# Kernel optimization log

Hardware: AMD Instinct MI355X
Metric: run time of the kernel (lower is better)

Reference implementation:

```python
import jax, jax.numpy as jnp
import numpy as np

B, S, D = 4, 2048, 512
H = 8
HD = D // H  # 64


def setup_inputs() -> dict:
    key = jax.random.key(0)
    k1, k2, k3 = jax.random.split(key, 3)
    x = jax.random.normal(k1, (B, S, D), dtype=jnp.float32)
    w_qkv = jax.random.normal(k2, (3 * D, D), dtype=jnp.float32) * (D ** -0.5)
    w_out = jax.random.normal(k3, (D, D), dtype=jnp.float32) * (D ** -0.5)
    return {"x": x, "w_qkv": w_qkv, "w_out": w_out}


def reference(x, w_qkv, w_out):
    b, s, d = x.shape
    # qkv projection (no bias), split into q,k,v
    qkv = jnp.einsum('bsd,ed->bse', x, w_qkv)  # [b, s, 3*d]
    q, k, v = jnp.split(qkv, 3, axis=2)
    # [b, s, h*hd] -> [b, h, s, hd]
    def to_heads(t):
        return t.reshape(b, s, H, HD).transpose(0, 2, 1, 3)
    q, k, v = to_heads(q), to_heads(k), to_heads(v)
    # NOTE: original module only scales by sqrt(head_dim) when mask is given;
    # with mask=None softmax is over raw QK^T scores.
    scores = jnp.einsum('bnid,bnjd->bnij', q, k)  # [b, h, s, s]
    attn = jax.nn.softmax(scores, axis=-1)
    o = jnp.einsum('bnij,bnjd->bnid', attn, v)  # [b, h, s, hd]
    o = o.transpose(0, 2, 1, 3).reshape(b, s, d)
    # dropout is identity (eval / drop_prob=0)
    return jnp.einsum('bsd,ed->bse', o, w_out)
```

## Files before the change

kernel.cpp:

```cpp
#include <hip/hip_runtime.h>
#include <hip/hip_bf16.h>

constexpr int B_  = 4;
constexpr int S_  = 2048;
constexpr int D_  = 512;
constexpr int H_  = 8;
constexpr int HD_ = 64;
constexpr int M_  = B_ * S_;

constexpr float LOG2E = 1.4426950408889634f;

typedef __attribute__((ext_vector_type(8))) short short8v;
typedef __attribute__((ext_vector_type(8))) _Float16 half8v;
typedef __attribute__((ext_vector_type(8))) unsigned short ushort8v;
typedef __attribute__((ext_vector_type(4))) float float4v;
typedef __attribute__((ext_vector_type(16))) float float16v;

__device__ __forceinline__ unsigned short f2bf(float x) {
    unsigned u = __builtin_bit_cast(unsigned, x);
    u += 0x7fffu + ((u >> 16) & 1u);
    return (unsigned short)(u >> 16);
}
__device__ __forceinline__ float bf2f(unsigned short h) {
    return __builtin_bit_cast(float, ((unsigned)h) << 16);
}
__device__ __forceinline__ unsigned short f2h(float x) {
    return __builtin_bit_cast(unsigned short, (_Float16)x);
}
__device__ __forceinline__ float fast_exp2(float x) {
#if __has_builtin(__builtin_amdgcn_exp2f)
    return __builtin_amdgcn_exp2f(x);
#else
    return exp2f(x);
#endif
}
__device__ __forceinline__ unsigned pack_bf16_trunc(float lo, float hi) {
    const unsigned ulo = __builtin_bit_cast(unsigned, lo);
    const unsigned uhi = __builtin_bit_cast(unsigned, hi);
#if __has_builtin(__builtin_amdgcn_perm)
    return __builtin_amdgcn_perm(uhi, ulo, 0x07060302u);
#else
    return (uhi & 0xffff0000u) | (ulo >> 16);
#endif
}
__device__ __forceinline__ void gload_lds16(const void* g, void* lds) {
    __builtin_amdgcn_global_load_lds((const __attribute__((address_space(1))) unsigned*)g,
                                     (__attribute__((address_space(3))) unsigned*)lds, 16, 0, 0);
}

__global__ __launch_bounds__(256) void prepass(const float* __restrict__ x,
                                               const float* __restrict__ wqkv,
                                               const float* __restrict__ wout,
                                               unsigned short* __restrict__ Xf,
                                               unsigned short* __restrict__ Wf,
                                               unsigned short* __restrict__ Wob) {
    const int bid = blockIdx.x, t = threadIdx.x;
    if (bid < 2048) {
        const int flat = bid * 256 + t;
        const int m = flat >> 6, c = (flat & 63) * 8;
        const float4 a = *(const float4*)&x[(size_t)m * 512 + c];
        const float4 b = *(const float4*)&x[(size_t)m * 512 + c + 4];
        const float v[8] = {a.x, a.y, a.z, a.w, b.x, b.y, b.z, b.w};
        ushort8v o;
#pragma unroll
        for (int i = 0; i < 8; ++i) o[i] = f2h(v[i]);
        *(ushort8v*)&Xf[(size_t)m * 512 + c] = o;
    } else if (bid < 2048 + 384) {
        const int flat = (bid - 2048) * 256 + t;
        const int e = flat >> 6, c = (flat & 63) * 8;
        const float4 a = *(const float4*)&wqkv[(size_t)e * 512 + c];
        const float4 b = *(const float4*)&wqkv[(size_t)e * 512 + c + 4];
        const float v[8] = {a.x, a.y, a.z, a.w, b.x, b.y, b.z, b.w};
        ushort8v o;
#pragma unroll
        for (int i = 0; i < 8; ++i) o[i] = f2h(v[i]);
        *(ushort8v*)&Wf[(size_t)e * 512 + c] = o;
    } else {
        const int flat = (bid - 2432) * 256 + t;
        const int e = flat >> 6, c = (flat & 63) * 8;
        const float4 a = *(const float4*)&wout[(size_t)e * 512 + c];
        const float4 b = *(const float4*)&wout[(size_t)e * 512 + c + 4];
        const float v[8] = {a.x, a.y, a.z, a.w, b.x, b.y, b.z, b.w};
        ushort8v o;
#pragma unroll
        for (int i = 0; i < 8; ++i) o[i] = f2bf(v[i]);
        *(ushort8v*)&Wob[(size_t)e * 512 + c] = o;
    }
}

__global__ __launch_bounds__(256, 2) void gemm_qkv(const unsigned short* __restrict__ Xf,
                                                   const unsigned short* __restrict__ Wf,
                                                   unsigned short* __restrict__ Qf,
                                                   unsigned short* __restrict__ KH,
                                                   unsigned short* __restrict__ VT) {
    __shared__ unsigned short Asm[2][128 * 64];
    __shared__ unsigned short Bsm[2][128 * 64];
    const int t = threadIdx.x, wv = t >> 6, lane = t & 63;
    const int fm = lane & 15, fq = lane >> 4;
    const int bid0 = blockIdx.x + 12 * blockIdx.y;
    const int xcd = bid0 & 7, ii = bid0 >> 3;
    const int x  = ii % 12;
    const int m0 = ((ii / 12) * 8 + xcd) * 128;
    const int slice = x >> 2;
    const int e0 = (x & 3) * 128;
    const bool vblk = (slice == 2);
    const int wrow = (wv >> 1) * 64, wcol = (wv & 1) * 64;

    const unsigned short* Bbase = Wf + (size_t)(e0 + slice * 512) * 512;

    const int srow = t >> 3;
    const int skb0 = t & 7;

    float4v acc[4][4];
#pragma unroll
    for (int i = 0; i < 4; ++i)
#pragma unroll
        for (int j = 0; j < 4; ++j) acc[i][j] = (float4v){0.f, 0.f, 0.f, 0.f};

#pragma unroll
    for (int i = 0; i < 4; ++i) {
        const int row = srow + 32 * i;
        const int kb = skb0 ^ (row & 7);
        gload_lds16(Xf + (size_t)(m0 + row) * 512 + kb * 8,
                    &Asm[0][(wv * 64 + 256 * i) * 8]);
        gload_lds16(Bbase + (size_t)row * 512 + kb * 8,
                    &Bsm[0][(wv * 64 + 256 * i) * 8]);
    }

    for (int kk = 0; kk < 8; ++kk) {
        __syncthreads();

        if (kk + 1 < 8) {
            const int k0n = (kk + 1) * 64;
            const int nbuf = (kk + 1) & 1;
#pragma unroll
            for (int i = 0; i < 4; ++i) {
                const int row = srow + 32 * i;
                const int kb = skb0 ^ (row & 7);
                gload_lds16(Xf + (size_t)(m0 + row) * 512 + k0n + kb * 8,
                            &Asm[nbuf][(wv * 64 + 256 * i) * 8]);
                gload_lds16(Bbase + (size_t)row * 512 + k0n + kb * 8,
                            &Bsm[nbuf][(wv * 64 + 256 * i) * 8]);
            }
        }

        const int buf = kk & 1;
#pragma unroll
        for (int ks = 0; ks < 2; ++ks) {
            half8v af[4], bf[4];
#pragma unroll
            for (int mt = 0; mt < 4; ++mt) {
                const int row = wrow + mt * 16 + fm;
                af[mt] = *(const half8v*)&Asm[buf][row * 64 + 8 * ((4 * ks + fq) ^ (row & 7))];
            }
#pragma unroll
            for (int nt = 0; nt < 4; ++nt) {
                const int row = wcol + nt * 16 + fm;
                bf[nt] = *(const half8v*)&Bsm[buf][row * 64 + 8 * ((4 * ks + fq) ^ (row & 7))];
            }
            if (vblk) {
#pragma unroll
                for (int mt = 0; mt < 4; ++mt)
#pragma unroll
                    for (int nt = 0; nt < 4; ++nt)
                        acc[mt][nt] = __builtin_amdgcn_mfma_f32_16x16x32_f16(bf[nt], af[mt], acc[mt][nt], 0, 0, 0);
            } else {
#pragma unroll
                for (int mt = 0; mt < 4; ++mt)
#pragma unroll
                    for (int nt = 0; nt < 4; ++nt)
                        acc[mt][nt] = __builtin_amdgcn_mfma_f32_16x16x32_f16(af[mt], bf[nt], acc[mt][nt], 0, 0, 0);
            }
        }
    }

    if (!vblk) {
        unsigned short* __restrict__ dst = (slice == 0) ? Qf : KH;
        const float sc = (slice == 0) ? LOG2E : 1.0f;
#pragma unroll
        for (int mt = 0; mt < 4; ++mt)
#pragma unroll
            for (int nt = 0; nt < 4; ++nt) {
                const int e = e0 + wcol + nt * 16 + fm;
                const int h = e >> 6, hd = e & 63;
#pragma unroll
                for (int r = 0; r < 4; ++r) {
                    const int m = m0 + wrow + mt * 16 + 4 * fq + r;
                    const int b = m >> 11, s = m & 2047;
                    dst[((size_t)(b * 8 + h) * 2048 + s) * 64 + hd] =
                        f2h(acc[mt][nt][r] * sc);
                }
            }
    } else {
#pragma unroll
        for (int nt = 0; nt < 4; ++nt)
#pragma unroll
            for (int r = 0; r < 4; ++r) {
                const int e = e0 + wcol + nt * 16 + 4 * fq + r;
                const int h = e >> 6, hd = e & 63;
#pragma unroll
                for (int mt = 0; mt < 4; ++mt) {
                    const int m = m0 + wrow + mt * 16 + fm;
                    const int b = m >> 11, s = m & 2047;
                    const int s2 = (s & ~12) | ((s & 4) << 1) | ((s & 8) >> 1);
                    VT[((size_t)(b * 8 + h) * 64 + hd) * 2048 + s2] = f2bf(acc[mt][nt][r]);
                }
            }
    }
}

__global__ __launch_bounds__(512, 1) void attn(const unsigned short* __restrict__ Qfp,
                                               const unsigned short* __restrict__ KHp,
                                               const unsigned short* __restrict__ VTp,
                                               unsigned short* __restrict__ OB) {
    __shared__ unsigned short Ks[2][64 * 64];
    __shared__ unsigned short Vs[2][64 * 64];
    const int t = threadIdx.x, wv = t >> 6, lane = t & 63;
    const int lq = lane & 31;
    const int hf2 = lane >> 5;
    const int bid0 = blockIdx.x + 8 * blockIdx.y;
    const int xcd = bid0 & 7, ii = bid0 >> 3;
    const int bh = (ii & 3) * 8 + xcd;
    const int q0 = (ii >> 2) * 256;

    const unsigned short* qfp = Qfp + (size_t)bh * S_ * 64;
    const unsigned short* kh  = KHp + (size_t)bh * S_ * 64;
    const unsigned short* vt  = VTp + (size_t)bh * 64 * S_;

    const int srow = t >> 3;
    const int skb0 = t & 7;
    const int kbs  = skb0 ^ (srow & 7);
    const int ldst = wv * 512 * 8;

#define STAGE_K(N, B) \
    gload_lds16(kh + (size_t)((N) * 64 + srow) * 64 + kbs * 8, &Ks[B][wv * 512])

#define STAGE_V(N, B) \
    gload_lds16(vt + (size_t)srow * S_ + (N) * 64 + kbs * 8, &Vs[B][wv * 512])

#define QK_STEP(SN, KR) do {                                                    \
    _Pragma("unroll")                                                           \
    for (int jb_ = 0; jb_ < 2; ++jb_)                                           \
        _Pragma("unroll")                                                       \
        for (int r_ = 0; r_ < 16; ++r_) SN[jb_][r_] = 0.f;                      \
    _Pragma("unroll")                                                           \
    for (int kk_ = 0; kk_ < 4; ++kk_)                                           \
        _Pragma("unroll")                                                       \
        for (int jb_ = 0; jb_ < 2; ++jb_) {                                     \
            const int row_ = jb_ * 32 + lq;                                     \
            const int cb_ = 2 * kk_ + hf2;                                      \
            const half8v kf_ = *(const half8v*)&Ks[KR][row_ * 64 + 8 * (cb_ ^ (row_ & 7))]; \
            SN[jb_] = __builtin_amdgcn_mfma_f32_32x32x16_f16(kf_, qf[kk_], SN[jb_], 0, 0, 0); \
        } } while (0)

#define SOFTMAX_PV(SC, VR) do {                                                 \
    unsigned pk_[2][4][2];                                                      \
    _Pragma("unroll")                                                           \
    for (int jb_ = 0; jb_ < 2; ++jb_)                                           \
        _Pragma("unroll")                                                       \
        for (int g_ = 0; g_ < 4; ++g_) {                                        \
            const float p0_ = fast_exp2(SC[jb_][4 * g_ + 0]);                   \
            const float p1_ = fast_exp2(SC[jb_][4 * g_ + 1]);                   \
            const float p2_ = fast_exp2(SC[jb_][4 * g_ + 2]);                   \
            const float p3_ = fast_exp2(SC[jb_][4 * g_ + 3]);                   \
            lsum += (p0_ + p1_) + (p2_ + p3_);                                  \
            pk_[jb_][g_][0] = pack_bf16_trunc(p0_, p1_);                        \
            pk_[jb_][g_][1] = pack_bf16_trunc(p2_, p3_);                        \
        }                                                                       \
    __builtin_amdgcn_s_setprio(1);                                              \
    _Pragma("unroll")                                                           \
    for (int jc_ = 0; jc_ < 4; ++jc_) {                                         \
        const int jb_ = jc_ >> 1, gg_ = (jc_ & 1) * 2;                          \
        const uint4 uu_ = {pk_[jb_][gg_][0], pk_[jb_][gg_][1],                  \
                           pk_[jb_][gg_ + 1][0], pk_[jb_][gg_ + 1][1]};         \
        const short8v pa_ = __builtin_bit_cast(short8v, uu_);                   \
        _Pragma("unroll")                                                       \
        for (int db_ = 0; db_ < 2; ++db_) {                                     \
            const int vrow_ = db_ * 32 + lq;                                    \
            const int cb_ = 2 * jc_ + hf2;                                      \
            const short8v vf_ = *(const short8v*)&Vs[VR][vrow_ * 64 + 8 * (cb_ ^ (vrow_ & 7))]; \
            accO[db_] = __builtin_amdgcn_mfma_f32_32x32x16_bf16(pa_, vf_, accO[db_], 0, 0, 0);  \
        }                                                                       \
    }                                                                           \
    __builtin_amdgcn_s_setprio(0);                                              \
} while (0)

    STAGE_K(0, 0);
    STAGE_V(0, 0);
    STAGE_K(1, 1);

    half8v qf[4];
    {
        const int qrow = q0 + wv * 32 + lq;
#pragma unroll
        for (int kk = 0; kk < 4; ++kk)
            qf[kk] = *(const half8v*)&qfp[(size_t)qrow * 64 + kk * 16 + hf2 * 8];
    }

    float16v accO[2];
#pragma unroll
    for (int db = 0; db < 2; ++db)
#pragma unroll
        for (int r = 0; r < 16; ++r) accO[db][r] = 0.f;
    float lsum = 0.f;

    float16v sA[2], sB[2];

    __syncthreads();
    QK_STEP(sA, 0);
    __syncthreads();

    for (int jt = 0; jt < 32; jt += 2) {
        if (jt + 2 < 32) STAGE_K(jt + 2, 0);
        STAGE_V(jt + 1, 1);
        QK_STEP(sB, 1);
        SOFTMAX_PV(sA, 0);
        __syncthreads();
        if (jt + 3 < 32) STAGE_K(jt + 3, 1);
        if (jt + 2 < 32) {
            STAGE_V(jt + 2, 0);
            QK_STEP(sA, 0);
        }
        SOFTMAX_PV(sB, 1);
        __syncthreads();
    }

#undef STAGE_K
#undef STAGE_V
#undef QK_STEP
#undef SOFTMAX_PV

    const float ls = lsum + __shfl_xor(lsum, 32);
    const float invl = 1.f / ls;

    const int b = bh >> 3, hh = bh & 7;
#pragma unroll
    for (int g = 0; g < 4; ++g)
#pragma unroll
        for (int r = 0; r < 4; ++r) {
            const int qrow = r + 8 * g + 4 * hf2;
            const float inv = __shfl(invl, qrow);
            const int q = q0 + wv * 32 + qrow;
#pragma unroll
            for (int db = 0; db < 2; ++db)
                OB[((size_t)(b * 2048 + q)) * 512 + hh * 64 + db * 32 + lq] =
                    f2bf(accO[db][4 * g + r] * inv);
        }
}

__global__ __launch_bounds__(256, 2) void gemm_out(const unsigned short* __restrict__ OB,
                                                   const unsigned short* __restrict__ Wob,
                                                   float* __restrict__ out) {
    __shared__ unsigned short Asm[2][128 * 64];
    __shared__ unsigned short Bsm[2][128 * 64];
    const int t = threadIdx.x, wv = t >> 6, lane = t & 63;
    const int fm = lane & 15, fq = lane >> 4;
    const int bid0 = blockIdx.x + 4 * blockIdx.y;
    const int xcd = bid0 & 7, ii = bid0 >> 3;
    const int e0 = (ii % 4) * 128;
    const int m0 = ((ii / 4) * 8 + xcd) * 128;
    const int wrow = (wv >> 1) * 64, wcol = (wv & 1) * 64;

    const int srow = t >> 3;
    const int skb0 = t & 7;

    float4v acc[4][4];
#pragma unroll
    for (int i = 0; i < 4; ++i)
#pragma unroll
        for (int j = 0; j < 4; ++j) acc[i][j] = (float4v){0.f, 0.f, 0.f, 0.f};

#pragma unroll
    for (int i = 0; i < 4; ++i) {
        const int row = srow + 32 * i;
        const int kb = skb0 ^ (row & 7);
        gload_lds16(OB + (size_t)(m0 + row) * 512 + kb * 8,
                    &Asm[0][(wv * 64 + 256 * i) * 8]);
        gload_lds16(Wob + (size_t)(e0 + row) * 512 + kb * 8,
                    &Bsm[0][(wv * 64 + 256 * i) * 8]);
    }

    for (int kk = 0; kk < 8; ++kk) {
        __syncthreads();
        if (kk + 1 < 8) {
            const int k0n = (kk + 1) * 64, nbuf = (kk + 1) & 1;
#pragma unroll
            for (int i = 0; i < 4; ++i) {
                const int row = srow + 32 * i;
                const int kb = skb0 ^ (row & 7);
                gload_lds16(OB + (size_t)(m0 + row) * 512 + k0n + kb * 8,
                            &Asm[nbuf][(wv * 64 + 256 * i) * 8]);
                gload_lds16(Wob + (size_t)(e0 + row) * 512 + k0n + kb * 8,
                            &Bsm[nbuf][(wv * 64 + 256 * i) * 8]);
            }
        }
        const int buf = kk & 1;
#pragma unroll
        for (int ks = 0; ks < 2; ++ks) {
            short8v af[4], bf[4];
#pragma unroll
            for (int mt = 0; mt < 4; ++mt) {
                const int row = wrow + mt * 16 + fm;
                af[mt] = *(const short8v*)&Asm[buf][row * 64 + 8 * ((4 * ks + fq) ^ (row & 7))];
            }
#pragma unroll
            for (int nt = 0; nt < 4; ++nt) {
                const int row = wcol + nt * 16 + fm;
                bf[nt] = *(const short8v*)&Bsm[buf][row * 64 + 8 * ((4 * ks + fq) ^ (row & 7))];
            }
#pragma unroll
            for (int mt = 0; mt < 4; ++mt)
#pragma unroll
                for (int nt = 0; nt < 4; ++nt)
                    acc[mt][nt] = __builtin_amdgcn_mfma_f32_16x16x32_bf16(af[mt], bf[nt], acc[mt][nt], 0, 0, 0);
        }
    }
#pragma unroll
    for (int mt = 0; mt < 4; ++mt)
#pragma unroll
        for (int nt = 0; nt < 4; ++nt)
#pragma unroll
            for (int r = 0; r < 4; ++r) {
                const int m = m0 + wrow + mt * 16 + 4 * fq + r;
                const int e = e0 + wcol + nt * 16 + fm;
                out[(size_t)m * 512 + e] = acc[mt][nt][r];
            }
}

extern "C" void kernel_launch(void* const* d_in, const int* in_sizes, int n_in,
                              void* d_out, int out_size, void* d_ws, size_t ws_size,
                              hipStream_t stream) {
    const float* x     = (const float*)d_in[0];
    const float* w_qkv = (const float*)d_in[1];
    const float* w_out = (const float*)d_in[2];
    float* out = (float*)d_out;

    char* p = (char*)d_ws;
    unsigned short* Xf  = (unsigned short*)p;  p += (size_t)M_ * 512 * 2;
    unsigned short* Wf  = (unsigned short*)p;  p += (size_t)1536 * 512 * 2;
    unsigned short* Wob = (unsigned short*)p;  p += (size_t)512 * 512 * 2;
    unsigned short* Qf  = (unsigned short*)p;  p += (size_t)32 * S_ * 64 * 2;
    unsigned short* KH  = (unsigned short*)p;  p += (size_t)32 * S_ * 64 * 2;
    unsigned short* VT  = (unsigned short*)p;  p += (size_t)32 * 64 * S_ * 2;
    unsigned short* OB  = Xf;

    prepass<<<2560, 256, 0, stream>>>(x, w_qkv, w_out, Xf, Wf, Wob);
    gemm_qkv<<<dim3(12, 64), 256, 0, stream>>>(Xf, Wf, Qf, KH, VT);
    attn<<<dim3(8, 32), 512, 0, stream>>>(Qf, KH, VT, OB);
    gemm_out<<<dim3(4, 64), 256, 0, stream>>>(OB, Wob, out);
}
```

Baseline: 140.6 us.

## Use 128-key tiles with double-buffered K/V and per-subtile QK-softmax-PV loop

Doubles the attention key tile from 64 to 128 rows, so there are half as many barrier-separated iterations, and stages K and V for the next tile together into the alternate buffer. The old schedule overlapped the QK of one tile with the softmax/PV of the previous one. It is replaced by a sequential loop over four 32-key subtiles within each tile. This cuts synchronisation count but drops the explicit cross-tile software pipelining, and LDS use doubles.

```diff
diff --git a/kernel.cpp b/kernel.cpp
--- a/kernel.cpp
+++ b/kernel.cpp
@@ -213,8 +213,8 @@
                                                const unsigned short* __restrict__ KHp,
                                                const unsigned short* __restrict__ VTp,
                                                unsigned short* __restrict__ OB) {
-    __shared__ unsigned short Ks[2][64 * 64];
-    __shared__ unsigned short Vs[2][64 * 64];
+    __shared__ unsigned short Ks[2][128 * 64];
+    __shared__ unsigned short Vs[2][64 * 128];
     const int t = threadIdx.x, wv = t >> 6, lane = t & 63;
     const int lq = lane & 31;
     const int hf2 = lane >> 5;
@@ -227,67 +227,26 @@
     const unsigned short* kh  = KHp + (size_t)bh * S_ * 64;
     const unsigned short* vt  = VTp + (size_t)bh * 64 * S_;
 
-    const int srow = t >> 3;
-    const int skb0 = t & 7;
-    const int kbs  = skb0 ^ (srow & 7);
-    const int ldst = wv * 512 * 8;
-
-#define STAGE_K(N, B) \
-    gload_lds16(kh + (size_t)((N) * 64 + srow) * 64 + kbs * 8, &Ks[B][wv * 512])
-
-#define STAGE_V(N, B) \
-    gload_lds16(vt + (size_t)srow * S_ + (N) * 64 + kbs * 8, &Vs[B][wv * 512])
-
-#define QK_STEP(SN, KR) do {                                                    \
+#define STAGE_K(N, B) do {                                                      \
     _Pragma("unroll")                                                           \
-    for (int jb_ = 0; jb_ < 2; ++jb_)                                           \
-        _Pragma("unroll")                                                       \
-        for (int r_ = 0; r_ < 16; ++r_) SN[jb_][r_] = 0.f;                      \
+    for (int i_ = 0; i_ < 2; ++i_) {                                            \
+        const int row_ = i_ * 64 + wv * 8 + (lane >> 3);                        \
+        const int kb_ = (lane & 7) ^ ((lane >> 3) & 7);                         \
+        gload_lds16(kh + (size_t)((N) * 128 + row_) * 64 + kb_ * 8,             \
+                    &Ks[B][(i_ * 512 + wv * 64) * 8]);                          \
+    } } while (0)
+
+#define STAGE_V(N, B) do {                                                      \
     _Pragma("unroll")                                                           \
-    for (int kk_ = 0; kk_ < 4; ++kk_)                                           \
-        _Pragma("unroll")                                                       \
-        for (int jb_ = 0; jb_ < 2; ++jb_) {                                     \
-            const int row_ = jb_ * 32 + lq;                                     \
-            const int cb_ = 2 * kk_ + hf2;                                      \
-            const half8v kf_ = *(const half8v*)&Ks[KR][row_ * 64 + 8 * (cb_ ^ (row_ & 7))]; \
-            SN[jb_] = __builtin_amdgcn_mfma_f32_32x32x16_f16(kf_, qf[kk_], SN[jb_], 0, 0, 0); \
-        } } while (0)
-
-#define SOFTMAX_PV(SC, VR) do {                                                 \
-    unsigned pk_[2][4][2];                                                      \
-    _Pragma("unroll")                                                           \
-    for (int jb_ = 0; jb_ < 2; ++jb_)                                           \
-        _Pragma("unroll")                                                       \
-        for (int g_ = 0; g_ < 4; ++g_) {                                        \
-            const float p0_ = fast_exp2(SC[jb_][4 * g_ + 0]);                   \
-            const float p1_ = fast_exp2(SC[jb_][4 * g_ + 1]);                   \
-            const float p2_ = fast_exp2(SC[jb_][4 * g_ + 2]);                   \
-            const float p3_ = fast_exp2(SC[jb_][4 * g_ + 3]);                   \
-            lsum += (p0_ + p1_) + (p2_ + p3_);                                  \
-            pk_[jb_][g_][0] = pack_bf16_trunc(p0_, p1_);                        \
-            pk_[jb_][g_][1] = pack_bf16_trunc(p2_, p3_);                        \
-        }                                                                       \
-    __builtin_amdgcn_s_setprio(1);                                              \
-    _Pragma("unroll")                                                           \
-    for (int jc_ = 0; jc_ < 4; ++jc_) {                                         \
-        const int jb_ = jc_ >> 1, gg_ = (jc_ & 1) * 2;                          \
-        const uint4 uu_ = {pk_[jb_][gg_][0], pk_[jb_][gg_][1],                  \
-                           pk_[jb_][gg_ + 1][0], pk_[jb_][gg_ + 1][1]};         \
-        const short8v pa_ = __builtin_bit_cast(short8v, uu_);                   \
-        _Pragma("unroll")                                                       \
-        for (int db_ = 0; db_ < 2; ++db_) {                                     \
-            const int vrow_ = db_ * 32 + lq;                                    \
-            const int cb_ = 2 * jc_ + hf2;                                      \
-            const short8v vf_ = *(const short8v*)&Vs[VR][vrow_ * 64 + 8 * (cb_ ^ (vrow_ & 7))]; \
-            accO[db_] = __builtin_amdgcn_mfma_f32_32x32x16_bf16(pa_, vf_, accO[db_], 0, 0, 0);  \
-        }                                                                       \
-    }                                                                           \
-    __builtin_amdgcn_s_setprio(0);                                              \
-} while (0)
+    for (int i_ = 0; i_ < 2; ++i_) {                                            \
+        const int row_ = i_ * 32 + wv * 4 + (lane >> 4);                        \
+        const int gc_ = (lane & 15) ^ (row_ & 7);                               \
+        gload_lds16(vt + (size_t)row_ * S_ + (N) * 128 + gc_ * 8,               \
+                    &Vs[B][(i_ * 512 + wv * 64) * 8]);                          \
+    } } while (0)
 
     STAGE_K(0, 0);
     STAGE_V(0, 0);
-    STAGE_K(1, 1);
 
     half8v qf[4];
     {
@@ -304,31 +263,64 @@
         for (int r = 0; r < 16; ++r) accO[db][r] = 0.f;
     float lsum = 0.f;
 
-    float16v sA[2], sB[2];
-
     __syncthreads();
-    QK_STEP(sA, 0);
-    __syncthreads();
-
-    for (int jt = 0; jt < 32; jt += 2) {
-        if (jt + 2 < 32) STAGE_K(jt + 2, 0);
-        STAGE_V(jt + 1, 1);
-        QK_STEP(sB, 1);
-        SOFTMAX_PV(sA, 0);
-        __syncthreads();
-        if (jt + 3 < 32) STAGE_K(jt + 3, 1);
-        if (jt + 2 < 32) {
-            STAGE_V(jt + 2, 0);
-            QK_STEP(sA, 0);
-        }
-        SOFTMAX_PV(sB, 1);
+
+    for (int n = 0; n < 16; ++n) {
+        const int buf = n & 1;
+        if (n + 1 < 16) {
+            STAGE_K(n + 1, buf ^ 1);
+            STAGE_V(n + 1, buf ^ 1);
+        }
+
+#pragma unroll
+        for (int jb = 0; jb < 4; ++jb) {
+            float16v sS;
+#pragma unroll
+            for (int r = 0; r < 16; ++r) sS[r] = 0.f;
+            __builtin_amdgcn_s_setprio(1);
+#pragma unroll
+            for (int kk = 0; kk < 4; ++kk) {
+                const int row = jb * 32 + lq;
+                const int cb = 2 * kk + hf2;
+                const half8v kf = *(const half8v*)&Ks[buf][row * 64 + 8 * (cb ^ (row & 7))];
+                sS = __builtin_amdgcn_mfma_f32_32x32x16_f16(kf, qf[kk], sS, 0, 0, 0);
+            }
+            __builtin_amdgcn_s_setprio(0);
+
+            unsigned pk[4][2];
+#pragma unroll
+            for (int g = 0; g < 4; ++g) {
+                const float p0 = fast_exp2(sS[4 * g + 0]);
+                const float p1 = fast_exp2(sS[4 * g + 1]);
+                const float p2 = fast_exp2(sS[4 * g + 2]);
+                const float p3 = fast_exp2(sS[4 * g + 3]);
+                lsum += (p0 + p1) + (p2 + p3);
+                pk[g][0] = pack_bf16_trunc(p0, p1);
+                pk[g][1] = pack_bf16_trunc(p2, p3);
+            }
+
+            __builtin_amdgcn_s_setprio(1);
+#pragma unroll
+            for (int w = 0; w < 2; ++w) {
+                const int jc = jb * 2 + w, gg = w * 2;
+                const uint4 uu = {pk[gg][0], pk[gg][1], pk[gg + 1][0], pk[gg + 1][1]};
+                const short8v pa = __builtin_bit_cast(short8v, uu);
+#pragma unroll
+                for (int db = 0; db < 2; ++db) {
+                    const int vrow = db * 32 + lq;
+                    const int cb2 = 2 * jc + hf2;
+                    const short8v vf = *(const short8v*)&Vs[buf][vrow * 128 + 8 * (cb2 ^ (vrow & 7))];
+                    accO[db] = __builtin_amdgcn_mfma_f32_32x32x16_bf16(pa, vf, accO[db], 0, 0, 0);
+                }
+            }
+            __builtin_amdgcn_s_setprio(0);
+        }
+
         __syncthreads();
     }
 
 #undef STAGE_K
 #undef STAGE_V
-#undef QK_STEP
-#undef SOFTMAX_PV
 
     const float ls = lsum + __shfl_xor(lsum, 32);
     const float invl = 1.f / ls;
```

Result: no change. 142.7 us (+1.5%).
